# Performance work log

Measured on AMD Instinct MI355X. Metric: run time of the kernel, lower is better.

The kernel has to match this reference:

```python
import jax, jax.numpy as jnp
import numpy as np

N_NODES, N_MSGS, MAX_NB = 35000, 80000, 6
IN_DIM, NODE_FDIM, H = 128, 128, 256
DEPTH = 5


def setup_inputs() -> dict:
    key = jax.random.key(0)
    ks = jax.random.split(key, 12)
    s_in = 1.0 / np.sqrt(IN_DIM + H)
    s_h = 1.0 / np.sqrt(H)
    s_o = 1.0 / np.sqrt(NODE_FDIM + H)
    return {
        "fnode": jax.random.normal(ks[0], (N_NODES, NODE_FDIM), jnp.float32),
        "fmess": jax.random.normal(ks[1], (N_MSGS, IN_DIM), jnp.float32),
        "agraph": jax.random.randint(ks[2], (N_NODES, MAX_NB), 0, N_MSGS),
        "bgraph": jax.random.randint(ks[3], (N_MSGS, MAX_NB), 0, N_MSGS),
        "mask": jnp.ones((N_NODES, 1), jnp.float32),
        # GRU params (stored as (in, out) so x @ W)
        "W_z": jax.random.uniform(ks[4], (IN_DIM + H, H), jnp.float32, -s_in, s_in),
        "b_z": jax.random.uniform(ks[5], (H,), jnp.float32, -s_in, s_in),
        "W_r": jax.random.uniform(ks[6], (IN_DIM, H), jnp.float32, -s_h, s_h),
        "U_r": jax.random.uniform(ks[7], (H, H), jnp.float32, -s_h, s_h),
        "b_ur": jax.random.uniform(ks[8], (H,), jnp.float32, -s_h, s_h),
        "W_h": jax.random.uniform(ks[9], (IN_DIM + H, H), jnp.float32, -s_in, s_in),
        "b_h": jax.random.uniform(ks[10], (H,), jnp.float32, -s_in, s_in),
        "W_o": jax.random.uniform(ks[11], (NODE_FDIM + H, H), jnp.float32, -s_o, s_o),
        "b_o": jnp.zeros((H,), jnp.float32),
    }


def _gru_message_passing(fmess, bgraph, W_z, b_z, W_r, U_r, b_ur, W_h, b_h):
    E = fmess.shape[0]
    # message 0 is the null message: its hidden state stays zero
    msg_mask = jnp.ones((E, 1), fmess.dtype).at[0, 0].set(0.0)
    rx = fmess @ W_r  # [E,H], loop-invariant
    h = jnp.zeros((E, H), fmess.dtype)

    def step(h, _):
        h_nei = h[bgraph]                      # [E, nb, H] gather
        sum_h = h_nei.sum(axis=1)              # [E, H]
        z = jax.nn.sigmoid(jnp.concatenate([fmess, sum_h], 1) @ W_z + b_z)
        r = jax.nn.sigmoid(rx[:, None, :] + h_nei @ U_r + b_ur)  # [E, nb, H]
        sum_gated = (r * h_nei).sum(axis=1)
        pre_h = jnp.tanh(jnp.concatenate([fmess, sum_gated], 1) @ W_h + b_h)
        h_new = ((1.0 - z) * sum_h + z * pre_h) * msg_mask
        return h_new, None

    h, _ = jax.lax.scan(step, h, None, length=DEPTH)
    return h


def reference(fnode, fmess, agraph, bgraph, mask,
              W_z, b_z, W_r, U_r, b_ur, W_h, b_h, W_o, b_o):
    h = _gru_message_passing(fmess, bgraph, W_z, b_z, W_r, U_r, b_ur, W_h, b_h)
    nei_message = h[agraph].sum(axis=1)        # [N, H]
    node_hiddens = jax.nn.relu(
        jnp.concatenate([fnode, nei_message], 1) @ W_o + b_o)
    return node_hiddens * mask, h
```

## Files before the change

kernel.cpp:

```cpp
#include <hip/hip_runtime.h>

#define H 256
#define NB 6
#define IN_DIM 128

typedef short s8v __attribute__((ext_vector_type(8)));
typedef float f4v __attribute__((ext_vector_type(4)));

__device__ __forceinline__ float fsigmoid(float x) {
    return 1.0f / (1.0f + __expf(-x));
}
__device__ __forceinline__ float ftanh(float x) {
    x = fminf(15.0f, fmaxf(-15.0f, x));
    float e = __expf(2.0f * x);
    return (e - 1.0f) / (e + 1.0f);
}
__device__ __forceinline__ unsigned short f2bf(float x) {
    unsigned u = __float_as_uint(x);
    u += 0x7fffu + ((u >> 16) & 1u);
    return (unsigned short)(u >> 16);
}
__device__ __forceinline__ float bf2f(unsigned short b) {
    return __uint_as_float(((unsigned)b) << 16);
}

__global__ __launch_bounds__(256) void wconv_kernel(
    const float* __restrict__ W, unsigned short* __restrict__ hi,
    unsigned short* __restrict__ lo, int K)
{
    const int i = blockIdx.x * 256 + threadIdx.x;
    if (i >= K * 256) return;
    const int n = i / K, k = i - n * K;
    const float x = W[(size_t)k * H + n];
    const unsigned short h = f2bf(x);
    hi[i] = h;
    lo[i] = f2bf(x - bf2f(h));
}

template<int EPI, bool A1BF, bool A2BF, bool OUTBF>
__global__ __launch_bounds__(256, 2) void mfma_gemm_kernel(
    const void* __restrict__ A1, int K1, const void* __restrict__ A2, int K2,
    const unsigned short* __restrict__ BThi, const unsigned short* __restrict__ BTlo,
    const float* __restrict__ bias, const float* __restrict__ mask,
    void* __restrict__ C, int M)
{
    const int KT = K1 + K2;
    __shared__ __align__(16) unsigned short Ah[128 * 40];
    __shared__ __align__(16) unsigned short Bh[128 * 40];
    __shared__ __align__(16) unsigned short Bl[128 * 40];

    const int tid = threadIdx.x;
    const int m0 = blockIdx.x * 128, n0 = blockIdx.y * 128;
    const int lane = tid & 63;
    const int w = tid >> 6;
    const int wmb = (w >> 1) * 64, wnb = (w & 1) * 64;
    const int lr = lane & 15;
    const int lkb = (lane >> 4) * 8;
    const int drb = (lane >> 4) * 4;
    const int ar = tid >> 1, kh = (tid & 1) * 16;

    f4v acc[4][4];
#pragma unroll
    for (int mi = 0; mi < 4; mi++)
#pragma unroll
        for (int ni = 0; ni < 4; ni++) acc[mi][ni] = (f4v){0.f, 0.f, 0.f, 0.f};

    for (int k0 = 0; k0 < KT; k0 += 32) {
        const void* src; int lda, kk; bool srcbf;
        if (k0 < K1) { src = A1; lda = K1; kk = k0;      srcbf = A1BF; }
        else         { src = A2; lda = K2; kk = k0 - K1; srcbf = A2BF; }
        const int grow = m0 + ar;
        if (grow < M) {
            if (srcbf) {
                const unsigned short* p = (const unsigned short*)src + (size_t)grow * lda + kk + kh;
                *(s8v*)&Ah[ar * 40 + kh]     = *(const s8v*)p;
                *(s8v*)&Ah[ar * 40 + kh + 8] = *(const s8v*)(p + 8);
            } else {
                const float* p = (const float*)src + (size_t)grow * lda + kk + kh;
#pragma unroll
                for (int i = 0; i < 4; i++) {
                    const float4 v = *(const float4*)(p + 4 * i);
                    *(ushort4*)&Ah[ar * 40 + kh + 4 * i] =
                        make_ushort4(f2bf(v.x), f2bf(v.y), f2bf(v.z), f2bf(v.w));
                }
            }
        }
        {
            const size_t bo = (size_t)(n0 + ar) * KT + k0 + kh;
            *(s8v*)&Bh[ar * 40 + kh]     = *(const s8v*)(BThi + bo);
            *(s8v*)&Bh[ar * 40 + kh + 8] = *(const s8v*)(BThi + bo + 8);
            *(s8v*)&Bl[ar * 40 + kh]     = *(const s8v*)(BTlo + bo);
            *(s8v*)&Bl[ar * 40 + kh + 8] = *(const s8v*)(BTlo + bo + 8);
        }
        __syncthreads();

        s8v av[4];
#pragma unroll
        for (int mi = 0; mi < 4; mi++)
            av[mi] = *(const s8v*)&Ah[(wmb + mi * 16 + lr) * 40 + lkb];
#pragma unroll
        for (int ni = 0; ni < 4; ni++) {
            const int cc = (wnb + ni * 16 + lr) * 40 + lkb;
            const s8v bv = *(const s8v*)&Bh[cc];
            const s8v bw = *(const s8v*)&Bl[cc];
#pragma unroll
            for (int mi = 0; mi < 4; mi++) {
                acc[mi][ni] = __builtin_amdgcn_mfma_f32_16x16x32_bf16(av[mi], bv, acc[mi][ni], 0, 0, 0);
                acc[mi][ni] = __builtin_amdgcn_mfma_f32_16x16x32_bf16(av[mi], bw, acc[mi][ni], 0, 0, 0);
            }
        }
        __syncthreads();
    }

#pragma unroll
    for (int mi = 0; mi < 4; mi++) {
#pragma unroll
        for (int ni = 0; ni < 4; ni++) {
#pragma unroll
            for (int r = 0; r < 4; r++) {
                const int row = m0 + wmb + mi * 16 + drb + r;
                if (row >= M) continue;
                const int col = n0 + wnb + ni * 16 + lr;
                float v = acc[mi][ni][r];
                if (EPI == 1) v = fmaxf(v + bias[col], 0.f) * mask[row];
                if (OUTBF) ((unsigned short*)C)[(size_t)row * H + col] = f2bf(v);
                else       ((float*)C)[(size_t)row * H + col] = v;
            }
        }
    }
}

template<bool STEP0, bool OUT32>
__global__ __launch_bounds__(256, 2) void mfma_update_kernel(
    const float* __restrict__ Xc,
    const float* __restrict__ smh, const float* __restrict__ smg,
    const unsigned short* __restrict__ WzThi, const unsigned short* __restrict__ WzTlo,
    const unsigned short* __restrict__ WhThi, const unsigned short* __restrict__ WhTlo,
    const float* __restrict__ b_z, const float* __restrict__ b_h,
    void* __restrict__ hout, int M, int grow0)
{
    __shared__ __align__(16) unsigned short Ah[128 * 40];
    __shared__ __align__(16) unsigned short Ch[128 * 40];
    __shared__ __align__(16) unsigned short Bzh[64 * 40];
    __shared__ __align__(16) unsigned short Bzl[64 * 40];
    __shared__ __align__(16) unsigned short Bhh[64 * 40];
    __shared__ __align__(16) unsigned short Bhl[64 * 40];

    const int tid = threadIdx.x;
    const int m0 = blockIdx.x * 128, n0 = blockIdx.y * 64;
    const int lane = tid & 63;
    const int w = tid >> 6;
    const int wmb = (w >> 1) * 64, wnb = (w & 1) * 32;
    const int lr = lane & 15;
    const int lkb = (lane >> 4) * 8;
    const int drb = (lane >> 4) * 4;
    const int ar = tid >> 1, kh = (tid & 1) * 16;
    const int bc = tid >> 2, kq = (tid & 3) * 8;

    f4v accz[4][2], acch[4][2];
#pragma unroll
    for (int mi = 0; mi < 4; mi++)
#pragma unroll
        for (int ni = 0; ni < 2; ni++) {
            accz[mi][ni] = (f4v){0.f, 0.f, 0.f, 0.f};
            acch[mi][ni] = (f4v){0.f, 0.f, 0.f, 0.f};
        }

    for (int k0 = 0; k0 < IN_DIM; k0 += 32) {
        const int grow = m0 + ar;
        if (grow < M) {
            const float* p = Xc + (size_t)grow * IN_DIM + k0 + kh;
#pragma unroll
            for (int i = 0; i < 4; i++) {
                const float4 v = *(const float4*)(p + 4 * i);
                *(ushort4*)&Ah[ar * 40 + kh + 4 * i] =
                    make_ushort4(f2bf(v.x), f2bf(v.y), f2bf(v.z), f2bf(v.w));
            }
        }
        {
            const size_t bo = (size_t)(n0 + bc) * 384 + k0 + kq;
            *(s8v*)&Bzh[bc * 40 + kq] = *(const s8v*)(WzThi + bo);
            *(s8v*)&Bzl[bc * 40 + kq] = *(const s8v*)(WzTlo + bo);
            *(s8v*)&Bhh[bc * 40 + kq] = *(const s8v*)(WhThi + bo);
            *(s8v*)&Bhl[bc * 40 + kq] = *(const s8v*)(WhTlo + bo);
        }
        __syncthreads();

        s8v av[4];
#pragma unroll
        for (int mi = 0; mi < 4; mi++)
            av[mi] = *(const s8v*)&Ah[(wmb + mi * 16 + lr) * 40 + lkb];
#pragma unroll
        for (int ni = 0; ni < 2; ni++) {
            const int cc = (wnb + ni * 16 + lr) * 40 + lkb;
            const s8v bzv = *(const s8v*)&Bzh[cc];
            const s8v bzw = *(const s8v*)&Bzl[cc];
            const s8v bhv = *(const s8v*)&Bhh[cc];
            const s8v bhw = *(const s8v*)&Bhl[cc];
#pragma unroll
            for (int mi = 0; mi < 4; mi++) {
                accz[mi][ni] = __builtin_amdgcn_mfma_f32_16x16x32_bf16(av[mi], bzv, accz[mi][ni], 0, 0, 0);
                accz[mi][ni] = __builtin_amdgcn_mfma_f32_16x16x32_bf16(av[mi], bzw, accz[mi][ni], 0, 0, 0);
                acch[mi][ni] = __builtin_amdgcn_mfma_f32_16x16x32_bf16(av[mi], bhv, acch[mi][ni], 0, 0, 0);
                acch[mi][ni] = __builtin_amdgcn_mfma_f32_16x16x32_bf16(av[mi], bhw, acch[mi][ni], 0, 0, 0);
            }
        }
        __syncthreads();
    }

    if (!STEP0) {
        for (int k0 = 0; k0 < H; k0 += 32) {
            const int grow = m0 + ar;
            if (grow < M) {
                const float* p1 = smh + (size_t)grow * H + k0 + kh;
                const float* p2 = smg + (size_t)grow * H + k0 + kh;
#pragma unroll
                for (int i = 0; i < 4; i++) {
                    const float4 v = *(const float4*)(p1 + 4 * i);
                    *(ushort4*)&Ah[ar * 40 + kh + 4 * i] =
                        make_ushort4(f2bf(v.x), f2bf(v.y), f2bf(v.z), f2bf(v.w));
                    const float4 u = *(const float4*)(p2 + 4 * i);
                    *(ushort4*)&Ch[ar * 40 + kh + 4 * i] =
                        make_ushort4(f2bf(u.x), f2bf(u.y), f2bf(u.z), f2bf(u.w));
                }
            }
            {
                const size_t bo = (size_t)(n0 + bc) * 384 + IN_DIM + k0 + kq;
                *(s8v*)&Bzh[bc * 40 + kq] = *(const s8v*)(WzThi + bo);
                *(s8v*)&Bzl[bc * 40 + kq] = *(const s8v*)(WzTlo + bo);
                *(s8v*)&Bhh[bc * 40 + kq] = *(const s8v*)(WhThi + bo);
                *(s8v*)&Bhl[bc * 40 + kq] = *(const s8v*)(WhTlo + bo);
            }
            __syncthreads();

            s8v av[4], cv[4];
#pragma unroll
            for (int mi = 0; mi < 4; mi++) {
                const int rr = (wmb + mi * 16 + lr) * 40 + lkb;
                av[mi] = *(const s8v*)&Ah[rr];
                cv[mi] = *(const s8v*)&Ch[rr];
            }
#pragma unroll
            for (int ni = 0; ni < 2; ni++) {
                const int cc = (wnb + ni * 16 + lr) * 40 + lkb;
                const s8v bzv = *(const s8v*)&Bzh[cc];
                const s8v bzw = *(const s8v*)&Bzl[cc];
                const s8v bhv = *(const s8v*)&Bhh[cc];
                const s8v bhw = *(const s8v*)&Bhl[cc];
#pragma unroll
                for (int mi = 0; mi < 4; mi++) {
                    accz[mi][ni] = __builtin_amdgcn_mfma_f32_16x16x32_bf16(av[mi], bzv, accz[mi][ni], 0, 0, 0);
                    accz[mi][ni] = __builtin_amdgcn_mfma_f32_16x16x32_bf16(av[mi], bzw, accz[mi][ni], 0, 0, 0);
                    acch[mi][ni] = __builtin_amdgcn_mfma_f32_16x16x32_bf16(cv[mi], bhv, acch[mi][ni], 0, 0, 0);
                    acch[mi][ni] = __builtin_amdgcn_mfma_f32_16x16x32_bf16(cv[mi], bhw, acch[mi][ni], 0, 0, 0);
                }
            }
            __syncthreads();
        }
    }

#pragma unroll
    for (int mi = 0; mi < 4; mi++) {
#pragma unroll
        for (int ni = 0; ni < 2; ni++) {
#pragma unroll
            for (int r = 0; r < 4; r++) {
                const int row = m0 + wmb + mi * 16 + drb + r;
                if (row >= M) continue;
                const int col = n0 + wnb + ni * 16 + lr;
                const float z = fsigmoid(accz[mi][ni][r] + b_z[col]);
                const float p = ftanh(acch[mi][ni][r] + b_h[col]);
                float o;
                if (STEP0) o = z * p;
                else       o = (1.f - z) * smh[(size_t)row * H + col] + z * p;
                if (grow0 + row == 0) o = 0.f;
                if (OUT32) ((float*)hout)[(size_t)row * H + col] = o;
                else       ((unsigned short*)hout)[(size_t)row * H + col] = f2bf(o);
            }
        }
    }
}

__global__ __launch_bounds__(256) void edge_kernel(
    const unsigned short* __restrict__ h, const unsigned short* __restrict__ g,
    const unsigned short* __restrict__ rx, const float* __restrict__ b_ur,
    const int* __restrict__ bgraph,
    float* __restrict__ smh, float* __restrict__ smg, int cc)
{
    const int e = blockIdx.x * 4 + (threadIdx.x >> 6);
    if (e >= cc) return;
    const int j = (threadIdx.x & 63) << 2;
    const ushort4 rv4 = *(const ushort4*)(rx + (size_t)e * H + j);
    const float4 bu = *(const float4*)(b_ur + j);
    const float r0 = bf2f(rv4.x) + bu.x, r1 = bf2f(rv4.y) + bu.y;
    const float r2 = bf2f(rv4.z) + bu.z, r3 = bf2f(rv4.w) + bu.w;
    float4 sh = make_float4(0.f, 0.f, 0.f, 0.f);
    float4 sg = make_float4(0.f, 0.f, 0.f, 0.f);
#pragma unroll
    for (int n = 0; n < NB; n++) {
        const int idx = bgraph[e * NB + n];
        const ushort4 hv4 = *(const ushort4*)(h + (size_t)idx * H + j);
        const ushort4 gv4 = *(const ushort4*)(g + (size_t)idx * H + j);
        const float h0 = bf2f(hv4.x), h1 = bf2f(hv4.y), h2 = bf2f(hv4.z), h3 = bf2f(hv4.w);
        sh.x += h0; sh.y += h1; sh.z += h2; sh.w += h3;
        sg.x = fmaf(fsigmoid(r0 + bf2f(gv4.x)), h0, sg.x);
        sg.y = fmaf(fsigmoid(r1 + bf2f(gv4.y)), h1, sg.y);
        sg.z = fmaf(fsigmoid(r2 + bf2f(gv4.z)), h2, sg.z);
        sg.w = fmaf(fsigmoid(r3 + bf2f(gv4.w)), h3, sg.w);
    }
    *(float4*)(smh + (size_t)e * H + j) = sh;
    *(float4*)(smg + (size_t)e * H + j) = sg;
}

__global__ __launch_bounds__(256) void node_gather_kernel(
    const float* __restrict__ hmsg, const int* __restrict__ agraph,
    unsigned short* __restrict__ nei, int N)
{
    const int v = blockIdx.x * 4 + (threadIdx.x >> 6);
    if (v >= N) return;
    const int j = (threadIdx.x & 63) << 2;
    float4 s = make_float4(0.f, 0.f, 0.f, 0.f);
#pragma unroll
    for (int n = 0; n < NB; n++) {
        const int idx = agraph[v * NB + n];
        const float4 hv = *(const float4*)(hmsg + (size_t)idx * H + j);
        s.x += hv.x; s.y += hv.y; s.z += hv.z; s.w += hv.w;
    }
    *(ushort4*)(nei + (size_t)v * H + j) =
        make_ushort4(f2bf(s.x), f2bf(s.y), f2bf(s.z), f2bf(s.w));
}

extern "C" void kernel_launch(void* const* d_in, const int* in_sizes, int n_in,
                              void* d_out, int out_size, void* d_ws, size_t ws_size,
                              hipStream_t stream)
{
    const float* fnode  = (const float*)d_in[0];
    const float* fmess  = (const float*)d_in[1];
    const int*   agraph = (const int*)  d_in[2];
    const int*   bgraph = (const int*)  d_in[3];
    const float* mask   = (const float*)d_in[4];
    const float* W_z    = (const float*)d_in[5];
    const float* b_z    = (const float*)d_in[6];
    const float* W_r    = (const float*)d_in[7];
    const float* U_r    = (const float*)d_in[8];
    const float* b_ur   = (const float*)d_in[9];
    const float* W_h    = (const float*)d_in[10];
    const float* b_h    = (const float*)d_in[11];
    const float* W_o    = (const float*)d_in[12];
    const float* b_o    = (const float*)d_in[13];

    const int N = in_sizes[0] / IN_DIM;
    const int E = in_sizes[1] / IN_DIM;
    const size_t EHu = (size_t)E * H;

    float* out_nodes = (float*)d_out;
    float* hA        = (float*)d_out + (size_t)N * H;
    unsigned short* hb0 = (unsigned short*)hA;
    unsigned short* hb1 = hb0 + EHu;

    unsigned short* wb = (unsigned short*)d_ws;
    unsigned short* wz_hi = wb;
    unsigned short* wz_lo = wb + 98304;
    unsigned short* wh_hi = wb + 196608;
    unsigned short* wh_lo = wb + 294912;
    unsigned short* wr_hi = wb + 393216;
    unsigned short* wr_lo = wb + 425984;
    unsigned short* ur_hi = wb + 458752;
    unsigned short* ur_lo = wb + 524288;
    unsigned short* wo_hi = wb + 589824;
    unsigned short* wo_lo = wb + 688128;
    unsigned short* rxb = wb + 786432;
    unsigned short* gb  = rxb + EHu;

    const size_t used_b = 786432ull * 2 + 2 * EHu * 2;
    float* fpool = (float*)((char*)d_ws + used_b);
    const size_t left_f = (ws_size - used_b) / 4;
    const int CH = (2 * EHu <= left_f) ? E : (E + 1) / 2;
    float* smh = fpool;
    float* smg = fpool + (size_t)CH * H;

    const dim3 blk(256);
    #define GG(M) dim3(((M) + 127) / 128, 2)
    #define GU(M) dim3(((M) + 127) / 128, 4)

    wconv_kernel<<<384, blk, 0, stream>>>(W_z, wz_hi, wz_lo, 384);
    wconv_kernel<<<384, blk, 0, stream>>>(W_h, wh_hi, wh_lo, 384);
    wconv_kernel<<<128, blk, 0, stream>>>(W_r, wr_hi, wr_lo, 128);
    wconv_kernel<<<256, blk, 0, stream>>>(U_r, ur_hi, ur_lo, 256);
    wconv_kernel<<<384, blk, 0, stream>>>(W_o, wo_hi, wo_lo, 384);

    mfma_gemm_kernel<0, false, false, true><<<GG(E), blk, 0, stream>>>(
        fmess, IN_DIM, nullptr, 0, wr_hi, wr_lo, nullptr, nullptr, rxb, E);
    mfma_update_kernel<true, false><<<GU(E), blk, 0, stream>>>(
        fmess, nullptr, nullptr, wz_hi, wz_lo, wh_hi, wh_lo, b_z, b_h, hb0, E, 0);

    unsigned short* hcur = hb0;
    unsigned short* hnxt = hb1;
    for (int t = 1; t < 5; t++) {
        mfma_gemm_kernel<0, true, false, true><<<GG(E), blk, 0, stream>>>(
            hcur, H, nullptr, 0, ur_hi, ur_lo, nullptr, nullptr, gb, E);
        for (int c0 = 0; c0 < E; c0 += CH) {
            const int cc = (E - c0 < CH) ? (E - c0) : CH;
            edge_kernel<<<(cc + 3) / 4, blk, 0, stream>>>(
                hcur, gb, rxb + (size_t)c0 * H, b_ur, bgraph + (size_t)c0 * NB,
                smh, smg, cc);
            if (t < 4)
                mfma_update_kernel<false, false><<<GU(cc), blk, 0, stream>>>(
                    fmess + (size_t)c0 * IN_DIM, smh, smg,
                    wz_hi, wz_lo, wh_hi, wh_lo, b_z, b_h,
                    hnxt + (size_t)c0 * H, cc, c0);
            else
                mfma_update_kernel<false, true><<<GU(cc), blk, 0, stream>>>(
                    fmess + (size_t)c0 * IN_DIM, smh, smg,
                    wz_hi, wz_lo, wh_hi, wh_lo, b_z, b_h,
                    hA + (size_t)c0 * H, cc, c0);
        }
        unsigned short* tmp = hcur; hcur = hnxt; hnxt = tmp;
    }

    node_gather_kernel<<<(N + 3) / 4, blk, 0, stream>>>(hA, agraph, gb, N);
    mfma_gemm_kernel<1, false, true, false><<<GG(N), blk, 0, stream>>>(
        fnode, IN_DIM, gb, H, wo_hi, wo_lo, b_o, mask, out_nodes, N);
    #undef GG
    #undef GU
}
```

Before: 1.605 ms.

## Hoist loop-invariant fmess projections out of GRU steps and store sums in bf16

The fmess@W_z, fmess@W_h and fmess@W_r projections, with their biases, are now computed once in a fused precompute kernel and stored as bf16. Each update step then runs only the K=256 hidden-state part of the GEMM, and step 0 becomes an elementwise kernel. The edge kernel writes its neighbour sums smh/smg as bf16 instead of fp32, which halves that traffic and lets the update kernel load them without converting. When everything fits in one chunk the hidden state is updated in place. The cost is extra bf16 rounding of the precomputed terms and of sum_h in the blend, which may reduce accuracy.

```diff
diff --git a/kernel.cpp b/kernel.cpp
--- a/kernel.cpp
+++ b/kernel.cpp
@@ -35,6 +35,128 @@
     const unsigned short h = f2bf(x);
     hi[i] = h;
     lo[i] = f2bf(x - bf2f(h));
+}
+
+__global__ __launch_bounds__(256, 2) void precompute3_kernel(
+    const float* __restrict__ X,
+    const unsigned short* __restrict__ WrH, const unsigned short* __restrict__ WrL,
+    const unsigned short* __restrict__ WzH, const unsigned short* __restrict__ WzL,
+    const unsigned short* __restrict__ WhH, const unsigned short* __restrict__ WhL,
+    const float* __restrict__ b_ur, const float* __restrict__ b_z,
+    const float* __restrict__ b_h,
+    unsigned short* __restrict__ rxb, unsigned short* __restrict__ zxb,
+    unsigned short* __restrict__ hxb, int M)
+{
+    __shared__ __align__(16) unsigned short Ah[128 * 40];
+    __shared__ __align__(16) unsigned short Brh[64 * 40];
+    __shared__ __align__(16) unsigned short Brl[64 * 40];
+    __shared__ __align__(16) unsigned short Bzh[64 * 40];
+    __shared__ __align__(16) unsigned short Bzl[64 * 40];
+    __shared__ __align__(16) unsigned short Bhh[64 * 40];
+    __shared__ __align__(16) unsigned short Bhl[64 * 40];
+
+    const int tid = threadIdx.x;
+    const int m0 = blockIdx.x * 128, n0 = blockIdx.y * 64;
+    const int lane = tid & 63;
+    const int w = tid >> 6;
+    const int wmb = (w >> 1) * 64, wnb = (w & 1) * 32;
+    const int lr = lane & 15;
+    const int lkb = (lane >> 4) * 8;
+    const int drb = (lane >> 4) * 4;
+    const int ar = tid >> 1, kh = (tid & 1) * 16;
+    const int bc = tid >> 2, kq = (tid & 3) * 8;
+
+    f4v ar_[4][2], az_[4][2], ah_[4][2];
+#pragma unroll
+    for (int mi = 0; mi < 4; mi++)
+#pragma unroll
+        for (int ni = 0; ni < 2; ni++) {
+            ar_[mi][ni] = (f4v){0.f, 0.f, 0.f, 0.f};
+            az_[mi][ni] = (f4v){0.f, 0.f, 0.f, 0.f};
+            ah_[mi][ni] = (f4v){0.f, 0.f, 0.f, 0.f};
+        }
+
+    for (int k0 = 0; k0 < IN_DIM; k0 += 32) {
+        const int grow = m0 + ar;
+        if (grow < M) {
+            const float* p = X + (size_t)grow * IN_DIM + k0 + kh;
+#pragma unroll
+            for (int i = 0; i < 4; i++) {
+                const float4 v = *(const float4*)(p + 4 * i);
+                *(ushort4*)&Ah[ar * 40 + kh + 4 * i] =
+                    make_ushort4(f2bf(v.x), f2bf(v.y), f2bf(v.z), f2bf(v.w));
+            }
+        }
+        {
+            const size_t bo = (size_t)(n0 + bc) * IN_DIM + k0 + kq;
+            *(s8v*)&Brh[bc * 40 + kq] = *(const s8v*)(WrH + bo);
+            *(s8v*)&Brl[bc * 40 + kq] = *(const s8v*)(WrL + bo);
+            *(s8v*)&Bzh[bc * 40 + kq] = *(const s8v*)(WzH + bo);
+            *(s8v*)&Bzl[bc * 40 + kq] = *(const s8v*)(WzL + bo);
+            *(s8v*)&Bhh[bc * 40 + kq] = *(const s8v*)(WhH + bo);
+            *(s8v*)&Bhl[bc * 40 + kq] = *(const s8v*)(WhL + bo);
+        }
+        __syncthreads();
+
+        s8v av[4];
+#pragma unroll
+        for (int mi = 0; mi < 4; mi++)
+            av[mi] = *(const s8v*)&Ah[(wmb + mi * 16 + lr) * 40 + lkb];
+#pragma unroll
+        for (int ni = 0; ni < 2; ni++) {
+            const int cc = (wnb + ni * 16 + lr) * 40 + lkb;
+            const s8v rv = *(const s8v*)&Brh[cc];
+            const s8v rw = *(const s8v*)&Brl[cc];
+            const s8v zv = *(const s8v*)&Bzh[cc];
+            const s8v zw = *(const s8v*)&Bzl[cc];
+            const s8v hv = *(const s8v*)&Bhh[cc];
+            const s8v hw = *(const s8v*)&Bhl[cc];
+#pragma unroll
+            for (int mi = 0; mi < 4; mi++) {
+                ar_[mi][ni] = __builtin_amdgcn_mfma_f32_16x16x32_bf16(av[mi], rv, ar_[mi][ni], 0, 0, 0);
+                ar_[mi][ni] = __builtin_amdgcn_mfma_f32_16x16x32_bf16(av[mi], rw, ar_[mi][ni], 0, 0, 0);
+                az_[mi][ni] = __builtin_amdgcn_mfma_f32_16x16x32_bf16(av[mi], zv, az_[mi][ni], 0, 0, 0);
+                az_[mi][ni] = __builtin_amdgcn_mfma_f32_16x16x32_bf16(av[mi], zw, az_[mi][ni], 0, 0, 0);
+                ah_[mi][ni] = __builtin_amdgcn_mfma_f32_16x16x32_bf16(av[mi], hv, ah_[mi][ni], 0, 0, 0);
+                ah_[mi][ni] = __builtin_amdgcn_mfma_f32_16x16x32_bf16(av[mi], hw, ah_[mi][ni], 0, 0, 0);
+            }
+        }
+        __syncthreads();
+    }
+
+#pragma unroll
+    for (int mi = 0; mi < 4; mi++) {
+#pragma unroll
+        for (int ni = 0; ni < 2; ni++) {
+#pragma unroll
+            for (int r = 0; r < 4; r++) {
+                const int row = m0 + wmb + mi * 16 + drb + r;
+                if (row >= M) continue;
+                const int col = n0 + wnb + ni * 16 + lr;
+                const size_t off = (size_t)row * H + col;
+                rxb[off] = f2bf(ar_[mi][ni][r] + b_ur[col]);
+                zxb[off] = f2bf(az_[mi][ni][r] + b_z[col]);
+                hxb[off] = f2bf(ah_[mi][ni][r] + b_h[col]);
+            }
+        }
+    }
+}
+
+__global__ __launch_bounds__(256) void step0_kernel(
+    const unsigned short* __restrict__ zxb, const unsigned short* __restrict__ hxb,
+    unsigned short* __restrict__ h, long total4)
+{
+    const long i = (long)blockIdx.x * 256 + threadIdx.x;
+    if (i >= total4) return;
+    const ushort4 z4 = ((const ushort4*)zxb)[i];
+    const ushort4 h4 = ((const ushort4*)hxb)[i];
+    ushort4 o;
+    o.x = f2bf(fsigmoid(bf2f(z4.x)) * ftanh(bf2f(h4.x)));
+    o.y = f2bf(fsigmoid(bf2f(z4.y)) * ftanh(bf2f(h4.y)));
+    o.z = f2bf(fsigmoid(bf2f(z4.z)) * ftanh(bf2f(h4.z)));
+    o.w = f2bf(fsigmoid(bf2f(z4.w)) * ftanh(bf2f(h4.w)));
+    if (i < H / 4) o = make_ushort4(0, 0, 0, 0);
+    ((ushort4*)h)[i] = o;
 }
 
 template<int EPI, bool A1BF, bool A2BF, bool OUTBF>
@@ -130,13 +252,12 @@
     }
 }
 
-template<bool STEP0, bool OUT32>
-__global__ __launch_bounds__(256, 2) void mfma_update_kernel(
-    const float* __restrict__ Xc,
-    const float* __restrict__ smh, const float* __restrict__ smg,
-    const unsigned short* __restrict__ WzThi, const unsigned short* __restrict__ WzTlo,
-    const unsigned short* __restrict__ WhThi, const unsigned short* __restrict__ WhTlo,
-    const float* __restrict__ b_z, const float* __restrict__ b_h,
+template<bool OUT32>
+__global__ __launch_bounds__(256, 2) void mfma_update2_kernel(
+    const unsigned short* __restrict__ smh, const unsigned short* __restrict__ smg,
+    const unsigned short* __restrict__ WzH, const unsigned short* __restrict__ WzL,
+    const unsigned short* __restrict__ WhH, const unsigned short* __restrict__ WhL,
+    const unsigned short* __restrict__ zxb, const unsigned short* __restrict__ hxb,
     void* __restrict__ hout, int M, int grow0)
 {
     __shared__ __align__(16) unsigned short Ah[128 * 40];
@@ -166,30 +287,32 @@
             acch[mi][ni] = (f4v){0.f, 0.f, 0.f, 0.f};
         }
 
-    for (int k0 = 0; k0 < IN_DIM; k0 += 32) {
+    for (int k0 = 0; k0 < H; k0 += 32) {
         const int grow = m0 + ar;
         if (grow < M) {
-            const float* p = Xc + (size_t)grow * IN_DIM + k0 + kh;
-#pragma unroll
-            for (int i = 0; i < 4; i++) {
-                const float4 v = *(const float4*)(p + 4 * i);
-                *(ushort4*)&Ah[ar * 40 + kh + 4 * i] =
-                    make_ushort4(f2bf(v.x), f2bf(v.y), f2bf(v.z), f2bf(v.w));
-            }
+            const unsigned short* p1 = smh + (size_t)grow * H + k0 + kh;
+            const unsigned short* p2 = smg + (size_t)grow * H + k0 + kh;
+            *(s8v*)&Ah[ar * 40 + kh]     = *(const s8v*)p1;
+            *(s8v*)&Ah[ar * 40 + kh + 8] = *(const s8v*)(p1 + 8);
+            *(s8v*)&Ch[ar * 40 + kh]     = *(const s8v*)p2;
+            *(s8v*)&Ch[ar * 40 + kh + 8] = *(const s8v*)(p2 + 8);
         }
         {
-            const size_t bo = (size_t)(n0 + bc) * 384 + k0 + kq;
-            *(s8v*)&Bzh[bc * 40 + kq] = *(const s8v*)(WzThi + bo);
-            *(s8v*)&Bzl[bc * 40 + kq] = *(const s8v*)(WzTlo + bo);
-            *(s8v*)&Bhh[bc * 40 + kq] = *(const s8v*)(WhThi + bo);
-            *(s8v*)&Bhl[bc * 40 + kq] = *(const s8v*)(WhTlo + bo);
+            const size_t bo = (size_t)(n0 + bc) * H + k0 + kq;
+            *(s8v*)&Bzh[bc * 40 + kq] = *(const s8v*)(WzH + bo);
+            *(s8v*)&Bzl[bc * 40 + kq] = *(const s8v*)(WzL + bo);
+            *(s8v*)&Bhh[bc * 40 + kq] = *(const s8v*)(WhH + bo);
+            *(s8v*)&Bhl[bc * 40 + kq] = *(const s8v*)(WhL + bo);
         }
         __syncthreads();
 
-        s8v av[4];
-#pragma unroll
-        for (int mi = 0; mi < 4; mi++)
-            av[mi] = *(const s8v*)&Ah[(wmb + mi * 16 + lr) * 40 + lkb];
+        s8v av[4], cv[4];
+#pragma unroll
+        for (int mi = 0; mi < 4; mi++) {
+            const int rr = (wmb + mi * 16 + lr) * 40 + lkb;
+            av[mi] = *(const s8v*)&Ah[rr];
+            cv[mi] = *(const s8v*)&Ch[rr];
+        }
 #pragma unroll
         for (int ni = 0; ni < 2; ni++) {
             const int cc = (wnb + ni * 16 + lr) * 40 + lkb;
@@ -201,62 +324,11 @@
             for (int mi = 0; mi < 4; mi++) {
                 accz[mi][ni] = __builtin_amdgcn_mfma_f32_16x16x32_bf16(av[mi], bzv, accz[mi][ni], 0, 0, 0);
                 accz[mi][ni] = __builtin_amdgcn_mfma_f32_16x16x32_bf16(av[mi], bzw, accz[mi][ni], 0, 0, 0);
-                acch[mi][ni] = __builtin_amdgcn_mfma_f32_16x16x32_bf16(av[mi], bhv, acch[mi][ni], 0, 0, 0);
-                acch[mi][ni] = __builtin_amdgcn_mfma_f32_16x16x32_bf16(av[mi], bhw, acch[mi][ni], 0, 0, 0);
+                acch[mi][ni] = __builtin_amdgcn_mfma_f32_16x16x32_bf16(cv[mi], bhv, acch[mi][ni], 0, 0, 0);
+                acch[mi][ni] = __builtin_amdgcn_mfma_f32_16x16x32_bf16(cv[mi], bhw, acch[mi][ni], 0, 0, 0);
             }
         }
         __syncthreads();
-    }
-
-    if (!STEP0) {
-        for (int k0 = 0; k0 < H; k0 += 32) {
-            const int grow = m0 + ar;
-            if (grow < M) {
-                const float* p1 = smh + (size_t)grow * H + k0 + kh;
-                const float* p2 = smg + (size_t)grow * H + k0 + kh;
-#pragma unroll
-                for (int i = 0; i < 4; i++) {
-                    const float4 v = *(const float4*)(p1 + 4 * i);
-                    *(ushort4*)&Ah[ar * 40 + kh + 4 * i] =
-                        make_ushort4(f2bf(v.x), f2bf(v.y), f2bf(v.z), f2bf(v.w));
-                    const float4 u = *(const float4*)(p2 + 4 * i);
-                    *(ushort4*)&Ch[ar * 40 + kh + 4 * i] =
-                        make_ushort4(f2bf(u.x), f2bf(u.y), f2bf(u.z), f2bf(u.w));
-                }
-            }
-            {
-                const size_t bo = (size_t)(n0 + bc) * 384 + IN_DIM + k0 + kq;
-                *(s8v*)&Bzh[bc * 40 + kq] = *(const s8v*)(WzThi + bo);
-                *(s8v*)&Bzl[bc * 40 + kq] = *(const s8v*)(WzTlo + bo);
-                *(s8v*)&Bhh[bc * 40 + kq] = *(const s8v*)(WhThi + bo);
-                *(s8v*)&Bhl[bc * 40 + kq] = *(const s8v*)(WhTlo + bo);
-            }
-            __syncthreads();
-
-            s8v av[4], cv[4];
-#pragma unroll
-            for (int mi = 0; mi < 4; mi++) {
-                const int rr = (wmb + mi * 16 + lr) * 40 + lkb;
-                av[mi] = *(const s8v*)&Ah[rr];
-                cv[mi] = *(const s8v*)&Ch[rr];
-            }
-#pragma unroll
-            for (int ni = 0; ni < 2; ni++) {
-                const int cc = (wnb + ni * 16 + lr) * 40 + lkb;
-                const s8v bzv = *(const s8v*)&Bzh[cc];
-                const s8v bzw = *(const s8v*)&Bzl[cc];
-                const s8v bhv = *(const s8v*)&Bhh[cc];
-                const s8v bhw = *(const s8v*)&Bhl[cc];
-#pragma unroll
-                for (int mi = 0; mi < 4; mi++) {
-                    accz[mi][ni] = __builtin_amdgcn_mfma_f32_16x16x32_bf16(av[mi], bzv, accz[mi][ni], 0, 0, 0);
-                    accz[mi][ni] = __builtin_amdgcn_mfma_f32_16x16x32_bf16(av[mi], bzw, accz[mi][ni], 0, 0, 0);
-                    acch[mi][ni] = __builtin_amdgcn_mfma_f32_16x16x32_bf16(cv[mi], bhv, acch[mi][ni], 0, 0, 0);
-                    acch[mi][ni] = __builtin_amdgcn_mfma_f32_16x16x32_bf16(cv[mi], bhw, acch[mi][ni], 0, 0, 0);
-                }
-            }
-            __syncthreads();
-        }
     }
 
 #pragma unroll
@@ -268,14 +340,13 @@
                 const int row = m0 + wmb + mi * 16 + drb + r;
                 if (row >= M) continue;
                 const int col = n0 + wnb + ni * 16 + lr;
-                const float z = fsigmoid(accz[mi][ni][r] + b_z[col]);
-                const float p = ftanh(acch[mi][ni][r] + b_h[col]);
-                float o;
-                if (STEP0) o = z * p;
-                else       o = (1.f - z) * smh[(size_t)row * H + col] + z * p;
+                const size_t off = (size_t)row * H + col;
+                const float z = fsigmoid(accz[mi][ni][r] + bf2f(zxb[off]));
+                const float p = ftanh(acch[mi][ni][r] + bf2f(hxb[off]));
+                float o = (1.f - z) * bf2f(smh[off]) + z * p;
                 if (grow0 + row == 0) o = 0.f;
-                if (OUT32) ((float*)hout)[(size_t)row * H + col] = o;
-                else       ((unsigned short*)hout)[(size_t)row * H + col] = f2bf(o);
+                if (OUT32) ((float*)hout)[off] = o;
+                else       ((unsigned short*)hout)[off] = f2bf(o);
             }
         }
     }
@@ -283,17 +354,14 @@
 
 __global__ __launch_bounds__(256) void edge_kernel(
     const unsigned short* __restrict__ h, const unsigned short* __restrict__ g,
-    const unsigned short* __restrict__ rx, const float* __restrict__ b_ur,
-    const int* __restrict__ bgraph,
-    float* __restrict__ smh, float* __restrict__ smg, int cc)
+    const unsigned short* __restrict__ rx, const int* __restrict__ bgraph,
+    unsigned short* __restrict__ smh, unsigned short* __restrict__ smg, int cc)
 {
     const int e = blockIdx.x * 4 + (threadIdx.x >> 6);
     if (e >= cc) return;
     const int j = (threadIdx.x & 63) << 2;
     const ushort4 rv4 = *(const ushort4*)(rx + (size_t)e * H + j);
-    const float4 bu = *(const float4*)(b_ur + j);
-    const float r0 = bf2f(rv4.x) + bu.x, r1 = bf2f(rv4.y) + bu.y;
-    const float r2 = bf2f(rv4.z) + bu.z, r3 = bf2f(rv4.w) + bu.w;
+    const float r0 = bf2f(rv4.x), r1 = bf2f(rv4.y), r2 = bf2f(rv4.z), r3 = bf2f(rv4.w);
     float4 sh = make_float4(0.f, 0.f, 0.f, 0.f);
     float4 sg = make_float4(0.f, 0.f, 0.f, 0.f);
 #pragma unroll
@@ -308,8 +376,10 @@
         sg.z = fmaf(fsigmoid(r2 + bf2f(gv4.z)), h2, sg.z);
         sg.w = fmaf(fsigmoid(r3 + bf2f(gv4.w)), h3, sg.w);
     }
-    *(float4*)(smh + (size_t)e * H + j) = sh;
-    *(float4*)(smg + (size_t)e * H + j) = sg;
+    *(ushort4*)(smh + (size_t)e * H + j) =
+        make_ushort4(f2bf(sh.x), f2bf(sh.y), f2bf(sh.z), f2bf(sh.w));
+    *(ushort4*)(smg + (size_t)e * H + j) =
+        make_ushort4(f2bf(sg.x), f2bf(sg.y), f2bf(sg.z), f2bf(sg.w));
 }
 
 __global__ __launch_bounds__(256) void node_gather_kernel(
@@ -359,60 +429,69 @@
     unsigned short* hb1 = hb0 + EHu;
 
     unsigned short* wb = (unsigned short*)d_ws;
-    unsigned short* wz_hi = wb;
-    unsigned short* wz_lo = wb + 98304;
-    unsigned short* wh_hi = wb + 196608;
-    unsigned short* wh_lo = wb + 294912;
-    unsigned short* wr_hi = wb + 393216;
-    unsigned short* wr_lo = wb + 425984;
-    unsigned short* ur_hi = wb + 458752;
-    unsigned short* ur_lo = wb + 524288;
-    unsigned short* wo_hi = wb + 589824;
-    unsigned short* wo_lo = wb + 688128;
+    unsigned short* wzx_hi = wb;
+    unsigned short* wzx_lo = wb + 32768;
+    unsigned short* whx_hi = wb + 65536;
+    unsigned short* whx_lo = wb + 98304;
+    unsigned short* wr_hi  = wb + 131072;
+    unsigned short* wr_lo  = wb + 163840;
+    unsigned short* wz2_hi = wb + 196608;
+    unsigned short* wz2_lo = wb + 262144;
+    unsigned short* wh2_hi = wb + 327680;
+    unsigned short* wh2_lo = wb + 393216;
+    unsigned short* ur_hi  = wb + 458752;
+    unsigned short* ur_lo  = wb + 524288;
+    unsigned short* wo_hi  = wb + 589824;
+    unsigned short* wo_lo  = wb + 688128;
     unsigned short* rxb = wb + 786432;
-    unsigned short* gb  = rxb + EHu;
-
-    const size_t used_b = 786432ull * 2 + 2 * EHu * 2;
-    float* fpool = (float*)((char*)d_ws + used_b);
-    const size_t left_f = (ws_size - used_b) / 4;
-    const int CH = (2 * EHu <= left_f) ? E : (E + 1) / 2;
-    float* smh = fpool;
-    float* smg = fpool + (size_t)CH * H;
+    unsigned short* zxb = rxb + EHu;
+    unsigned short* hxb = zxb + EHu;
+    unsigned short* gb  = hxb + EHu;
+    unsigned short* smh = gb + EHu;
+
+    const size_t ws_u = ws_size / 2;
+    const size_t base_u = 786432 + 4 * EHu;
+    const int CH = (base_u + 2 * EHu <= ws_u) ? E : E / 2;
+    unsigned short* smg = smh + (size_t)CH * H;
 
     const dim3 blk(256);
-    #define GG(M) dim3(((M) + 127) / 128, 2)
-    #define GU(M) dim3(((M) + 127) / 128, 4)
-
-    wconv_kernel<<<384, blk, 0, stream>>>(W_z, wz_hi, wz_lo, 384);
-    wconv_kernel<<<384, blk, 0, stream>>>(W_h, wh_hi, wh_lo, 384);
-    wconv_kernel<<<128, blk, 0, stream>>>(W_r, wr_hi, wr_lo, 128);
-    wconv_kernel<<<256, blk, 0, stream>>>(U_r, ur_hi, ur_lo, 256);
-    wconv_kernel<<<384, blk, 0, stream>>>(W_o, wo_hi, wo_lo, 384);
-
-    mfma_gemm_kernel<0, false, false, true><<<GG(E), blk, 0, stream>>>(
-        fmess, IN_DIM, nullptr, 0, wr_hi, wr_lo, nullptr, nullptr, rxb, E);
-    mfma_update_kernel<true, false><<<GU(E), blk, 0, stream>>>(
-        fmess, nullptr, nullptr, wz_hi, wz_lo, wh_hi, wh_lo, b_z, b_h, hb0, E, 0);
+    #define GG(M)  dim3(((M) + 127) / 128, 2)
+    #define GU(M)  dim3(((M) + 127) / 128, 4)
+
+    wconv_kernel<<<128, blk, 0, stream>>>(W_z,            wzx_hi, wzx_lo, 128);
+    wconv_kernel<<<128, blk, 0, stream>>>(W_h,            whx_hi, whx_lo, 128);
+    wconv_kernel<<<128, blk, 0, stream>>>(W_r,            wr_hi,  wr_lo,  128);
+    wconv_kernel<<<256, blk, 0, stream>>>(W_z + 128 * H,  wz2_hi, wz2_lo, 256);
+    wconv_kernel<<<256, blk, 0, stream>>>(W_h + 128 * H,  wh2_hi, wh2_lo, 256);
+    wconv_kernel<<<256, blk, 0, stream>>>(U_r,            ur_hi,  ur_lo,  256);
+    wconv_kernel<<<384, blk, 0, stream>>>(W_o,            wo_hi,  wo_lo,  384);
+
+    precompute3_kernel<<<GU(E), blk, 0, stream>>>(
+        fmess, wr_hi, wr_lo, wzx_hi, wzx_lo, whx_hi, whx_lo,
+        b_ur, b_z, b_h, rxb, zxb, hxb, E);
+
+    step0_kernel<<<(int)((EHu / 4 + 255) / 256), blk, 0, stream>>>(
+        zxb, hxb, hb0, (long)(EHu / 4));
 
     unsigned short* hcur = hb0;
-    unsigned short* hnxt = hb1;
+    unsigned short* hnxt = (CH == E) ? hb0 : hb1;
     for (int t = 1; t < 5; t++) {
         mfma_gemm_kernel<0, true, false, true><<<GG(E), blk, 0, stream>>>(
             hcur, H, nullptr, 0, ur_hi, ur_lo, nullptr, nullptr, gb, E);
         for (int c0 = 0; c0 < E; c0 += CH) {
             const int cc = (E - c0 < CH) ? (E - c0) : CH;
             edge_kernel<<<(cc + 3) / 4, blk, 0, stream>>>(
-                hcur, gb, rxb + (size_t)c0 * H, b_ur, bgraph + (size_t)c0 * NB,
+                hcur, gb, rxb + (size_t)c0 * H, bgraph + (size_t)c0 * NB,
                 smh, smg, cc);
             if (t < 4)
-                mfma_update_kernel<false, false><<<GU(cc), blk, 0, stream>>>(
-                    fmess + (size_t)c0 * IN_DIM, smh, smg,
-                    wz_hi, wz_lo, wh_hi, wh_lo, b_z, b_h,
+                mfma_update2_kernel<false><<<GU(cc), blk, 0, stream>>>(
+                    smh, smg, wz2_hi, wz2_lo, wh2_hi, wh2_lo,
+                    zxb + (size_t)c0 * H, hxb + (size_t)c0 * H,
                     hnxt + (size_t)c0 * H, cc, c0);
             else
-                mfma_update_kernel<false, true><<<GU(cc), blk, 0, stream>>>(
-                    fmess + (size_t)c0 * IN_DIM, smh, smg,
-                    wz_hi, wz_lo, wh_hi, wh_lo, b_z, b_h,
+                mfma_update2_kernel<true><<<GU(cc), blk, 0, stream>>>(
+                    smh, smg, wz2_hi, wz2_lo, wh2_hi, wh2_lo,
+                    zxb + (size_t)c0 * H, hxb + (size_t)c0 * H,
                     hA + (size_t)c0 * H, cc, c0);
         }
         unsigned short* tmp = hcur; hcur = hnxt; hnxt = tmp;
```

After: 1.359 ms. 15.3% less time.
